# Performance work log

Hardware: AMD Instinct MI355X
Metric: run time of the kernel (lower is better)

The kernel has to match this reference:

```python
import jax, jax.numpy as jnp
import numpy as np

B, D, T = 8, 1024, 512
HID, NH, NL = 256, 4, 2
OUT = HID // NH  # 64 per-head dim
ALPHA = 0.2      # leaky relu slope
EPS = 1e-5       # layernorm eps


def setup_inputs() -> dict:
    key = jax.random.key(0)
    ks = jax.random.split(key, 10)
    X_obs = jax.random.normal(ks[0], (B, D, T), dtype=jnp.float32)
    mask = (jax.random.uniform(ks[1], (B, D, T)) < 0.8).astype(jnp.float32)
    W_in = jax.random.normal(ks[2], (2 * T, HID), dtype=jnp.float32) * (1.0 / np.sqrt(2 * T))
    b_in = jnp.zeros((HID,), dtype=jnp.float32)
    gat_W = jax.random.normal(ks[3], (NL, NH, HID, OUT), dtype=jnp.float32) * (1.0 / np.sqrt(HID))
    gat_a = jax.random.normal(ks[4], (NL, NH, 2 * OUT), dtype=jnp.float32) * 0.1
    ln_g = jnp.ones((NL, HID), dtype=jnp.float32)
    ln_b = jnp.zeros((NL, HID), dtype=jnp.float32)
    W_out = jax.random.normal(ks[5], (HID, T), dtype=jnp.float32) * (1.0 / np.sqrt(HID))
    b_out = jnp.zeros((T,), dtype=jnp.float32)
    return dict(X_obs=X_obs, mask=mask, W_in=W_in, b_in=b_in, gat_W=gat_W,
                gat_a=gat_a, ln_g=ln_g, ln_b=ln_b, W_out=W_out, b_out=b_out)


def _layer_norm(x, g, b):
    mu = jnp.mean(x, axis=-1, keepdims=True)
    var = jnp.mean((x - mu) ** 2, axis=-1, keepdims=True)
    return (x - mu) * jax.lax.rsqrt(var + EPS) * g + b


def _gat_forward(X_obs, mask, W_in, b_in, gat_W, gat_a, ln_g, ln_b, W_out, b_out):
    # mean-impute per (d, t) position across batch
    obs_sum = jnp.sum(X_obs * mask, axis=0, keepdims=True)
    obs_cnt = jnp.sum(mask, axis=0, keepdims=True)
    pos_mean = obs_sum / (obs_cnt + 1e-10)
    X_mean = X_obs * mask + (1.0 - mask) * pos_mean

    x = jnp.concatenate([X_mean, mask], axis=-1)       # (B, D, 2T)
    h = x @ W_in + b_in                                 # (B, N, HID)

    for l in range(NL):
        Wl = gat_W[l]                                   # (H, HID, OUT)
        a_left = gat_a[l, :, :OUT]                      # (H, OUT)
        a_right = gat_a[l, :, OUT:]                     # (H, OUT)
        hW = jnp.einsum('bnd,hde->bhne', h, Wl)         # (B, H, N, OUT)
        # e_ij = leakyrelu(a_left . h_i + a_right . h_j) -- avoids O(N^2 * 2d) concat
        s_l = jnp.einsum('bhne,he->bhn', hW, a_left)
        s_r = jnp.einsum('bhne,he->bhn', hW, a_right)
        e = jax.nn.leaky_relu(s_l[..., :, None] + s_r[..., None, :], ALPHA)  # (B,H,N,N)
        attn = jax.nn.softmax(e, axis=-1)
        head_out = jnp.einsum('bhnm,bhme->bhne', attn, hW)                   # (B,H,N,OUT)
        h_new = jnp.transpose(head_out, (0, 2, 1, 3)).reshape(h.shape[0], h.shape[1], HID)
        h = _layer_norm(h + h_new, ln_g[l], ln_b[l])

    return h @ W_out + b_out                            # (B, D, T)


def reference(X_obs, mask, W_in, b_in, gat_W, gat_a, ln_g, ln_b, W_out, b_out):
    return _gat_forward(X_obs, mask, W_in, b_in, gat_W, gat_a, ln_g, ln_b, W_out, b_out)
```

## Files before the change

### kernel.cpp

```cpp
#include <hip/hip_runtime.h>
#include <hip/hip_bf16.h>

constexpr int B_   = 8;
constexpr int D_   = 1024;
constexpr int T_   = 512;
constexpr int HID_ = 256;
constexpr int NH_  = 4;
constexpr int NL_  = 2;
constexpr float ALPHA_ = 0.2f;
constexpr float EPS_   = 1e-5f;
constexpr float LOG2E_ = 1.4426950408889634f;
constexpr int OUT_ = 64;
constexpr int M_ = B_ * D_;
constexpr int DT_ = D_ * T_;
constexpr int KIN_ = 2 * T_;

typedef __attribute__((ext_vector_type(8))) short short8;
typedef __attribute__((ext_vector_type(4))) float floatx4;

__device__ __forceinline__ unsigned short f2bf(float f) {
    unsigned int u = __float_as_uint(f);
    unsigned int r = u + 0x7fffu + ((u >> 16) & 1u);
    return (unsigned short)(r >> 16);
}
__device__ __forceinline__ float bf2f(unsigned short u) {
    return __uint_as_float((unsigned int)u << 16);
}
__device__ __forceinline__ unsigned int kenc(float f) {
    unsigned int u = __float_as_uint(f);
    return (u & 0x80000000u) ? ~u : (u | 0x80000000u);
}
__device__ __forceinline__ float kdec(unsigned int k) {
    unsigned int u = (k & 0x80000000u) ? (k ^ 0x80000000u) : ~k;
    return __uint_as_float(u);
}

__global__ __launch_bounds__(256) void prep_k(const float* __restrict__ X,
                                              const float* __restrict__ Mk,
                                              const float* __restrict__ W_in,
                                              const float* __restrict__ gatW,
                                              const float* __restrict__ W_out,
                                              unsigned short* __restrict__ Ain,
                                              unsigned short* __restrict__ Wt_in,
                                              unsigned short* __restrict__ Wcat,
                                              unsigned short* __restrict__ WtO,
                                              unsigned int* __restrict__ rmaxkey) {
    int bx = blockIdx.x;
    if (bx < 512) {
        int idx4 = (bx * 256 + threadIdx.x) * 4;
        int t = idx4 & (T_ - 1);
        int d = idx4 >> 9;
        float4 x[B_], m[B_];
        float4 s = {0, 0, 0, 0}, c = {0, 0, 0, 0};
#pragma unroll
        for (int b = 0; b < B_; b++) {
            x[b] = *(const float4*)&X[(size_t)b * DT_ + idx4];
            m[b] = *(const float4*)&Mk[(size_t)b * DT_ + idx4];
            s.x += x[b].x * m[b].x; s.y += x[b].y * m[b].y;
            s.z += x[b].z * m[b].z; s.w += x[b].w * m[b].w;
            c.x += m[b].x; c.y += m[b].y; c.z += m[b].z; c.w += m[b].w;
        }
        float4 pm;
        pm.x = s.x / (c.x + 1e-10f); pm.y = s.y / (c.y + 1e-10f);
        pm.z = s.z / (c.z + 1e-10f); pm.w = s.w / (c.w + 1e-10f);
#pragma unroll
        for (int b = 0; b < B_; b++) {
            size_t row = (size_t)b * D_ + d;
            ushort4 xm, mk;
            xm.x = f2bf(x[b].x * m[b].x + (1.f - m[b].x) * pm.x);
            xm.y = f2bf(x[b].y * m[b].y + (1.f - m[b].y) * pm.y);
            xm.z = f2bf(x[b].z * m[b].z + (1.f - m[b].z) * pm.z);
            xm.w = f2bf(x[b].w * m[b].w + (1.f - m[b].w) * pm.w);
            mk.x = f2bf(m[b].x); mk.y = f2bf(m[b].y);
            mk.z = f2bf(m[b].z); mk.w = f2bf(m[b].w);
            *(ushort4*)&Ain[row * KIN_ + t]      = xm;
            *(ushort4*)&Ain[row * KIN_ + T_ + t] = mk;
        }
    } else {
        int idx = (bx - 512) * 256 + threadIdx.x;
        if (idx < 64) rmaxkey[idx] = 0u;
        if (idx < 262144) {
            int n = idx >> 10, k = idx & 1023;
            Wt_in[idx] = f2bf(W_in[(size_t)k * HID_ + n]);
        } else if (idx < 393216) {
            int j = idx - 262144;
            int l = j >> 16, n = (j >> 8) & 255, k = j & 255;
            int h = n >> 6, e = n & 63;
            Wcat[j] = f2bf(gatW[(((size_t)(l * NH_ + h) * HID_) + k) * OUT_ + e]);
        } else {
            int j = idx - 393216;
            int n = j >> 8, k = j & 255;
            WtO[j] = f2bf(W_out[(size_t)k * T_ + n]);
        }
    }
}

template <int MODE>
__global__ __launch_bounds__(256) void gemm_bf16_k(
        const unsigned short* __restrict__ A,
        const unsigned short* __restrict__ Bt,
        const float* __restrict__ bias,
        float* __restrict__ C,
        unsigned short* __restrict__ Cb,
        const float* __restrict__ ga,
        float* __restrict__ s_l,
        float* __restrict__ s_r,
        unsigned int* __restrict__ rmaxkey,
        int Nsz, int Ksz) {
    __shared__ __align__(16) unsigned short As[2][64 * 72];
    __shared__ __align__(16) unsigned short Bs[2][64 * 72];
    int tid = threadIdx.x;
    int wave = tid >> 6, lane = tid & 63;
    int q = lane >> 4, r16 = lane & 15;
    int rowbase = blockIdx.y * 64;
    int colbase = blockIdx.x * 64;

    int srow = tid >> 3, sk = (tid & 7) * 8;
    const unsigned short* Ap0 = A + (size_t)(rowbase + srow) * Ksz + sk;
    const unsigned short* Ap1 = A + (size_t)(rowbase + srow + 32) * Ksz + sk;
    const unsigned short* Bp0 = Bt + (size_t)(colbase + srow) * Ksz + sk;
    const unsigned short* Bp1 = Bt + (size_t)(colbase + srow + 32) * Ksz + sk;
    int la0 = srow * 72 + sk, la1 = (srow + 32) * 72 + sk;

    floatx4 acc[4];
#pragma unroll
    for (int i = 0; i < 4; i++) acc[i] = (floatx4)0.f;

    uint4 pa0 = *(const uint4*)Ap0, pa1 = *(const uint4*)Ap1;
    uint4 pb0 = *(const uint4*)Bp0, pb1 = *(const uint4*)Bp1;
    *(uint4*)&As[0][la0] = pa0;
    *(uint4*)&As[0][la1] = pa1;
    *(uint4*)&Bs[0][la0] = pb0;
    *(uint4*)&Bs[0][la1] = pb1;

    int nk = Ksz >> 6;
    for (int it = 0; it < nk; it++) {
        int cur = it & 1;
        __syncthreads();
        if (it + 1 < nk) {
            int kt = (it + 1) << 6;
            pa0 = *(const uint4*)(Ap0 + kt);
            pa1 = *(const uint4*)(Ap1 + kt);
            pb0 = *(const uint4*)(Bp0 + kt);
            pb1 = *(const uint4*)(Bp1 + kt);
        }
#pragma unroll
        for (int t = 0; t < 2; t++) {
            short8 a = *(const short8*)&As[cur][(wave * 16 + r16) * 72 + t * 32 + q * 8];
#pragma unroll
            for (int ni = 0; ni < 4; ni++) {
                short8 b = *(const short8*)&Bs[cur][(ni * 16 + r16) * 72 + t * 32 + q * 8];
                acc[ni] = __builtin_amdgcn_mfma_f32_16x16x32_bf16(a, b, acc[ni], 0, 0, 0);
            }
        }
        if (it + 1 < nk) {
            int nxt = cur ^ 1;
            *(uint4*)&As[nxt][la0] = pa0;
            *(uint4*)&As[nxt][la1] = pa1;
            *(uint4*)&Bs[nxt][la0] = pb0;
            *(uint4*)&Bs[nxt][la1] = pb1;
        }
    }
    if constexpr (MODE == 2) {
        int bhh = ((rowbase >> 10) << 2) + blockIdx.x;
        int nb = (rowbase & (D_ - 1)) + wave * 16;
#pragma unroll
        for (int ni = 0; ni < 4; ni++) {
            int e = ni * 16 + r16;
            ushort4 pk;
            pk.x = f2bf(acc[ni][0]);
            pk.y = f2bf(acc[ni][1]);
            pk.z = f2bf(acc[ni][2]);
            pk.w = f2bf(acc[ni][3]);
            *(ushort4*)&Cb[((size_t)(bhh * 64 + e) << 10) + nb + q * 4] = pk;
        }
        const float* gab = ga + blockIdx.x * 2 * OUT_;
        float al4[4], ar4[4];
#pragma unroll
        for (int ni = 0; ni < 4; ni++) {
            al4[ni] = gab[ni * 16 + r16];
            ar4[ni] = gab[OUT_ + ni * 16 + r16];
        }
        float slv[4], srv[4];
#pragma unroll
        for (int rr = 0; rr < 4; rr++) {
            float s1 = 0.f, s2 = 0.f;
#pragma unroll
            for (int ni = 0; ni < 4; ni++) {
                s1 += acc[ni][rr] * al4[ni];
                s2 += acc[ni][rr] * ar4[ni];
            }
            slv[rr] = s1;
            srv[rr] = s2;
        }
#pragma unroll
        for (int off = 1; off < 16; off <<= 1) {
#pragma unroll
            for (int rr = 0; rr < 4; rr++) {
                slv[rr] += __shfl_xor(slv[rr], off, 64);
                srv[rr] += __shfl_xor(srv[rr], off, 64);
            }
        }
        {
            int rsel = r16 & 3;
            float sv = (rsel == 0) ? slv[0] : (rsel == 1) ? slv[1] : (rsel == 2) ? slv[2] : slv[3];
            float rv = (rsel == 0) ? srv[0] : (rsel == 1) ? srv[1] : (rsel == 2) ? srv[2] : srv[3];
            int n = nb + q * 4 + rsel;
            if (r16 < 4)                 s_l[bhh * D_ + n] = sv;
            else if (r16 >= 8 && r16 < 12) s_r[bhh * D_ + n] = rv;
        }
        float mx = fmaxf(fmaxf(srv[0], srv[1]), fmaxf(srv[2], srv[3]));
        mx = fmaxf(mx, __shfl_xor(mx, 16, 64));
        mx = fmaxf(mx, __shfl_xor(mx, 32, 64));
        if (lane == 0) atomicMax(&rmaxkey[bhh], kenc(mx));
    } else {
#pragma unroll
        for (int rr = 0; rr < 4; rr++) {
            int row = rowbase + wave * 16 + q * 4 + rr;
#pragma unroll
            for (int ni = 0; ni < 4; ni++) {
                int col = colbase + ni * 16 + r16;
                float v = acc[ni][rr] + (bias ? bias[col] : 0.f);
                if constexpr (MODE == 0) C[(size_t)row * Nsz + col] = v;
                else                     Cb[(size_t)row * Nsz + col] = f2bf(v);
            }
        }
    }
}

__global__ __launch_bounds__(256) void attn_k(const unsigned short* __restrict__ hwT,
                                              const float* __restrict__ sl_g,
                                              const float* __restrict__ sr_g,
                                              const unsigned int* __restrict__ rmaxkey,
                                              float* __restrict__ pacc,
                                              float* __restrict__ pden) {
    int bh = blockIdx.x;
    int b = bh >> 2, h = bh & 3;
    int half = blockIdx.z;
    int mb = half * 512;
    int tid = threadIdx.x;
    int wave = tid >> 6, lane = tid & 63;
    int q = lane >> 4, r16 = lane & 15;

    __shared__ float srs[512];
    __shared__ __align__(16) unsigned short Vt[2][64][136];

    {
        float2 sv = *(const float2*)&sr_g[bh * D_ + mb + tid * 2];
        sv.x *= LOG2E_; sv.y *= LOG2E_;
        *(float2*)&srs[tid * 2] = sv;
    }

    float rm = kdec(rmaxkey[bh]) * LOG2E_;
    int row0 = blockIdx.y * 64 + wave * 16;
    float sl = sl_g[bh * D_ + row0 + r16] * LOG2E_;
    float xm = sl + rm;
    float Mn = fmaxf(xm, ALPHA_ * xm);

    floatx4 acc[4];
#pragma unroll
    for (int i = 0; i < 4; i++) acc[i] = (floatx4)0.f;
    float dsum = 0.f;

    const unsigned short* vbase = hwT + ((size_t)(bh * 64) << 10) + mb;
    int se[4], sp[4];
#pragma unroll
    for (int i = 0; i < 4; i++) {
        int s = tid + i * 256;
        se[i] = s >> 4;
        sp[i] = (s & 15) * 8;
    }

    uint4 pre[4];
#pragma unroll
    for (int i = 0; i < 4; i++)
        pre[i] = *(const uint4*)&vbase[((size_t)se[i] << 10) + sp[i]];
#pragma unroll
    for (int i = 0; i < 4; i++)
        *(uint4*)&Vt[0][se[i]][sp[i]] = pre[i];
    __syncthreads();

    for (int c = 0; c < 4; c++) {
        int cur = c & 1;
        if (c < 3) {
            int mo = (c + 1) * 128;
#pragma unroll
            for (int i = 0; i < 4; i++)
                pre[i] = *(const uint4*)&vbase[((size_t)se[i] << 10) + mo + sp[i]];
        }
#pragma unroll
        for (int kk = 0; kk < 128; kk += 32) {
            int m0 = c * 128 + kk + q * 8;
            float4 s0 = *(const float4*)&srs[m0];
            float4 s1 = *(const float4*)&srs[m0 + 4];
            float sr8[8] = {s0.x, s0.y, s0.z, s0.w, s1.x, s1.y, s1.z, s1.w};
            float p[8];
#pragma unroll
            for (int j = 0; j < 8; j++) {
                float x = sl + sr8[j];
                float e = fmaxf(x, ALPHA_ * x);
                float pj = exp2f(e - Mn);
                dsum += pj;
                p[j] = pj;
            }
            union { unsigned int u[4]; short8 s8; } cv;
#pragma unroll
            for (int j = 0; j < 4; j++) {
                unsigned int lo = (__float_as_uint(p[2 * j]) + 0x8000u) >> 16;
                unsigned int hi = (__float_as_uint(p[2 * j + 1]) + 0x8000u) & 0xffff0000u;
                cv.u[j] = hi | lo;
            }
#pragma unroll
            for (int ni = 0; ni < 4; ni++) {
                short8 bfr = *(const short8*)&Vt[cur][ni * 16 + r16][kk + q * 8];
                acc[ni] = __builtin_amdgcn_mfma_f32_16x16x32_bf16(cv.s8, bfr, acc[ni], 0, 0, 0);
            }
        }
        if (c < 3) {
#pragma unroll
            for (int i = 0; i < 4; i++)
                *(uint4*)&Vt[cur ^ 1][se[i]][sp[i]] = pre[i];
        }
        __syncthreads();
    }
    dsum += __shfl_xor(dsum, 16);
    dsum += __shfl_xor(dsum, 32);
    size_t gr0 = (size_t)b * D_ + row0;
    if (lane < 16) pden[((size_t)half * M_ + gr0 + r16) * NH_ + h] = dsum;
#pragma unroll
    for (int rr = 0; rr < 4; rr++) {
        size_t grow = gr0 + q * 4 + rr;
#pragma unroll
        for (int ni = 0; ni < 4; ni++) {
            pacc[((size_t)half * M_ + grow) * HID_ + h * OUT_ + ni * 16 + r16] = acc[ni][rr];
        }
    }
}

__global__ __launch_bounds__(256) void addln_k(unsigned short* __restrict__ hbf,
                                               const float* __restrict__ pacc,
                                               const float* __restrict__ pden,
                                               const float* __restrict__ g,
                                               const float* __restrict__ bb) {
    int wave = threadIdx.x >> 6, lane = threadIdx.x & 63;
    size_t row = (size_t)blockIdx.x * 4 + wave;
    ushort4 hb = *(const ushort4*)&hbf[row * HID_ + lane * 4];
    float4 p0 = *(const float4*)&pacc[row * HID_ + lane * 4];
    float4 p1 = *(const float4*)&pacc[((size_t)M_ + row) * HID_ + lane * 4];
    int hh = lane >> 4;
    float den = pden[row * NH_ + hh] + pden[((size_t)M_ + row) * NH_ + hh];
    float inv = 1.f / den;
    float4 v = {bf2f(hb.x) + (p0.x + p1.x) * inv, bf2f(hb.y) + (p0.y + p1.y) * inv,
                bf2f(hb.z) + (p0.z + p1.z) * inv, bf2f(hb.w) + (p0.w + p1.w) * inv};
    float s = v.x + v.y + v.z + v.w;
#pragma unroll
    for (int off = 1; off < 64; off <<= 1) s += __shfl_xor(s, off, 64);
    float mu = s * (1.f / HID_);
    float4 d = {v.x - mu, v.y - mu, v.z - mu, v.w - mu};
    float s2 = d.x * d.x + d.y * d.y + d.z * d.z + d.w * d.w;
#pragma unroll
    for (int off = 1; off < 64; off <<= 1) s2 += __shfl_xor(s2, off, 64);
    float rs = rsqrtf(s2 * (1.f / HID_) + EPS_);
    float4 gg = *(const float4*)&g[lane * 4];
    float4 bbv = *(const float4*)&bb[lane * 4];
    ushort4 pk;
    pk.x = f2bf(d.x * rs * gg.x + bbv.x);
    pk.y = f2bf(d.y * rs * gg.y + bbv.y);
    pk.z = f2bf(d.z * rs * gg.z + bbv.z);
    pk.w = f2bf(d.w * rs * gg.w + bbv.w);
    *(ushort4*)&hbf[row * HID_ + lane * 4] = pk;
}

extern "C" void kernel_launch(void* const* d_in, const int* in_sizes, int n_in,
                              void* d_out, int out_size, void* d_ws, size_t ws_size,
                              hipStream_t stream) {
    const float* X_obs = (const float*)d_in[0];
    const float* mask  = (const float*)d_in[1];
    const float* W_in  = (const float*)d_in[2];
    const float* b_in  = (const float*)d_in[3];
    const float* gat_W = (const float*)d_in[4];
    const float* gat_a = (const float*)d_in[5];
    const float* ln_g  = (const float*)d_in[6];
    const float* ln_b  = (const float*)d_in[7];
    const float* W_out = (const float*)d_in[8];
    const float* b_out = (const float*)d_in[9];
    float* out = (float*)d_out;

    char* base = (char*)d_ws;
    unsigned short* Ain  = (unsigned short*)base;
    unsigned short* hwT  = (unsigned short*)base;
    float* pacc = (float*)(base + (4u << 20));
    float* pden = (float*)(base + (20u << 20));
    unsigned short* hbf   = (unsigned short*)(base + (21u << 20));
    unsigned short* Wt_in = (unsigned short*)(base + (25u << 20));
    unsigned short* Wcat  = Wt_in + (size_t)HID_ * KIN_;
    unsigned short* WtO   = Wcat + (size_t)NL_ * HID_ * HID_;
    float* slb = (float*)(WtO + (size_t)T_ * HID_);
    float* srb = slb + B_ * NH_ * D_;
    unsigned int* rmaxkey = (unsigned int*)(srb + B_ * NH_ * D_);

    prep_k<<<2560, 256, 0, stream>>>(X_obs, mask, W_in, gat_W, W_out,
                                     Ain, Wt_in, Wcat, WtO, rmaxkey);

    gemm_bf16_k<1><<<dim3(HID_ / 64, M_ / 64), 256, 0, stream>>>(
        Ain, Wt_in, b_in, nullptr, hbf, nullptr, nullptr, nullptr, nullptr,
        HID_, KIN_);

    for (int l = 0; l < NL_; l++) {
        gemm_bf16_k<2><<<dim3(HID_ / 64, M_ / 64), 256, 0, stream>>>(
            hbf, Wcat + (size_t)l * HID_ * HID_, nullptr, nullptr, hwT,
            gat_a + (size_t)l * NH_ * 2 * OUT_, slb, srb, rmaxkey + l * 32,
            HID_, HID_);
        attn_k<<<dim3(B_ * NH_, D_ / 64, 2), 256, 0, stream>>>(
            hwT, slb, srb, rmaxkey + l * 32, pacc, pden);
        addln_k<<<M_ / 4, 256, 0, stream>>>(hbf, pacc, pden,
                                            ln_g + (size_t)l * HID_,
                                            ln_b + (size_t)l * HID_);
    }

    gemm_bf16_k<0><<<dim3(T_ / 64, M_ / 64), 256, 0, stream>>>(
        hbf, WtO, b_out, out, nullptr, nullptr, nullptr, nullptr, nullptr,
        T_, HID_);
}
```

Baseline: 219.2 us.

## Fuse residual add and layernorm into following GEMM prologue, drop addln kernel

Removes the separate add+layernorm kernel. Each GAT layer's residual+LN is now computed in the prologue of the next GEMM (the layer-2 projection and the output projection), with the normalized tile staged straight into shared memory. The K=256 GEMMs now load the whole A and B tiles into LDS at once instead of double-buffering. Each column block recomputes LN for its rows, which is redundant work (4x or 8x), and only blockIdx.x==0 writes the normalized h out to a ping-pong buffer.

```diff
diff --git a/kernel.cpp b/kernel.cpp
--- a/kernel.cpp
+++ b/kernel.cpp
@@ -95,18 +95,11 @@
     }
 }
 
-template <int MODE>
-__global__ __launch_bounds__(256) void gemm_bf16_k(
+__global__ __launch_bounds__(256) void gemm1_k(
         const unsigned short* __restrict__ A,
         const unsigned short* __restrict__ Bt,
         const float* __restrict__ bias,
-        float* __restrict__ C,
-        unsigned short* __restrict__ Cb,
-        const float* __restrict__ ga,
-        float* __restrict__ s_l,
-        float* __restrict__ s_r,
-        unsigned int* __restrict__ rmaxkey,
-        int Nsz, int Ksz) {
+        unsigned short* __restrict__ Cb) {
     __shared__ __align__(16) unsigned short As[2][64 * 72];
     __shared__ __align__(16) unsigned short Bs[2][64 * 72];
     int tid = threadIdx.x;
@@ -116,10 +109,10 @@
     int colbase = blockIdx.x * 64;
 
     int srow = tid >> 3, sk = (tid & 7) * 8;
-    const unsigned short* Ap0 = A + (size_t)(rowbase + srow) * Ksz + sk;
-    const unsigned short* Ap1 = A + (size_t)(rowbase + srow + 32) * Ksz + sk;
-    const unsigned short* Bp0 = Bt + (size_t)(colbase + srow) * Ksz + sk;
-    const unsigned short* Bp1 = Bt + (size_t)(colbase + srow + 32) * Ksz + sk;
+    const unsigned short* Ap0 = A + (size_t)(rowbase + srow) * KIN_ + sk;
+    const unsigned short* Ap1 = A + (size_t)(rowbase + srow + 32) * KIN_ + sk;
+    const unsigned short* Bp0 = Bt + (size_t)(colbase + srow) * KIN_ + sk;
+    const unsigned short* Bp1 = Bt + (size_t)(colbase + srow + 32) * KIN_ + sk;
     int la0 = srow * 72 + sk, la1 = (srow + 32) * 72 + sk;
 
     floatx4 acc[4];
@@ -133,11 +126,10 @@
     *(uint4*)&Bs[0][la0] = pb0;
     *(uint4*)&Bs[0][la1] = pb1;
 
-    int nk = Ksz >> 6;
-    for (int it = 0; it < nk; it++) {
+    for (int it = 0; it < 16; it++) {
         int cur = it & 1;
         __syncthreads();
-        if (it + 1 < nk) {
+        if (it + 1 < 16) {
             int kt = (it + 1) << 6;
             pa0 = *(const uint4*)(Ap0 + kt);
             pa1 = *(const uint4*)(Ap1 + kt);
@@ -153,7 +145,7 @@
                 acc[ni] = __builtin_amdgcn_mfma_f32_16x16x32_bf16(a, b, acc[ni], 0, 0, 0);
             }
         }
-        if (it + 1 < nk) {
+        if (it + 1 < 16) {
             int nxt = cur ^ 1;
             *(uint4*)&As[nxt][la0] = pa0;
             *(uint4*)&As[nxt][la1] = pa1;
@@ -161,7 +153,109 @@
             *(uint4*)&Bs[nxt][la1] = pb1;
         }
     }
-    if constexpr (MODE == 2) {
+#pragma unroll
+    for (int rr = 0; rr < 4; rr++) {
+        int row = rowbase + wave * 16 + q * 4 + rr;
+#pragma unroll
+        for (int ni = 0; ni < 4; ni++) {
+            int col = colbase + ni * 16 + r16;
+            Cb[(size_t)row * HID_ + col] = f2bf(acc[ni][rr] + bias[col]);
+        }
+    }
+}
+
+template <bool LNF, int EPI>
+__global__ __launch_bounds__(256) void gemm_small_k(
+        const unsigned short* __restrict__ Ah,
+        const float* __restrict__ pacc,
+        const float* __restrict__ pden,
+        const float* __restrict__ lng,
+        const float* __restrict__ lnb,
+        unsigned short* __restrict__ hOut,
+        const unsigned short* __restrict__ Bt,
+        const float* __restrict__ bias,
+        float* __restrict__ C,
+        unsigned short* __restrict__ hwT,
+        const float* __restrict__ ga,
+        float* __restrict__ s_l,
+        float* __restrict__ s_r,
+        unsigned int* __restrict__ rmaxkey,
+        int Nsz) {
+    constexpr int STR = 264;
+    __shared__ __align__(16) unsigned short As[64 * STR];
+    __shared__ __align__(16) unsigned short Bs[64 * STR];
+    int tid = threadIdx.x;
+    int wave = tid >> 6, lane = tid & 63;
+    int q = lane >> 4, r16 = lane & 15;
+    int rowbase = blockIdx.y * 64;
+    int colbase = blockIdx.x * 64;
+
+#pragma unroll
+    for (int i = 0; i < 8; i++) {
+        int s = tid + i * 256;
+        int n = s >> 5, part = s & 31;
+        *(uint4*)&Bs[n * STR + part * 8] =
+            *(const uint4*)&Bt[(size_t)(colbase + n) * HID_ + part * 8];
+    }
+    if constexpr (!LNF) {
+#pragma unroll
+        for (int i = 0; i < 8; i++) {
+            int s = tid + i * 256;
+            int r = s >> 5, part = s & 31;
+            *(uint4*)&As[r * STR + part * 8] =
+                *(const uint4*)&Ah[(size_t)(rowbase + r) * HID_ + part * 8];
+        }
+    } else {
+        float4 gg = *(const float4*)&lng[lane * 4];
+        float4 bbv = *(const float4*)&lnb[lane * 4];
+        int hh = lane >> 4;
+        bool wr = (hOut != nullptr) && (blockIdx.x == 0);
+#pragma unroll 4
+        for (int i = 0; i < 16; i++) {
+            size_t row = (size_t)rowbase + wave * 16 + i;
+            ushort4 hb = *(const ushort4*)&Ah[row * HID_ + lane * 4];
+            float4 p0 = *(const float4*)&pacc[row * HID_ + lane * 4];
+            float4 p1 = *(const float4*)&pacc[((size_t)M_ + row) * HID_ + lane * 4];
+            float den = pden[row * NH_ + hh] + pden[((size_t)M_ + row) * NH_ + hh];
+            float inv = 1.f / den;
+            float4 v = {bf2f(hb.x) + (p0.x + p1.x) * inv,
+                        bf2f(hb.y) + (p0.y + p1.y) * inv,
+                        bf2f(hb.z) + (p0.z + p1.z) * inv,
+                        bf2f(hb.w) + (p0.w + p1.w) * inv};
+            float s = v.x + v.y + v.z + v.w;
+#pragma unroll
+            for (int off = 1; off < 64; off <<= 1) s += __shfl_xor(s, off, 64);
+            float mu = s * (1.f / HID_);
+            float4 d = {v.x - mu, v.y - mu, v.z - mu, v.w - mu};
+            float s2 = d.x * d.x + d.y * d.y + d.z * d.z + d.w * d.w;
+#pragma unroll
+            for (int off = 1; off < 64; off <<= 1) s2 += __shfl_xor(s2, off, 64);
+            float rs = rsqrtf(s2 * (1.f / HID_) + EPS_);
+            ushort4 pk;
+            pk.x = f2bf(d.x * rs * gg.x + bbv.x);
+            pk.y = f2bf(d.y * rs * gg.y + bbv.y);
+            pk.z = f2bf(d.z * rs * gg.z + bbv.z);
+            pk.w = f2bf(d.w * rs * gg.w + bbv.w);
+            *(ushort4*)&As[(wave * 16 + i) * STR + lane * 4] = pk;
+            if (wr) *(ushort4*)&hOut[row * HID_ + lane * 4] = pk;
+        }
+    }
+    __syncthreads();
+
+    floatx4 acc[4];
+#pragma unroll
+    for (int i = 0; i < 4; i++) acc[i] = (floatx4)0.f;
+#pragma unroll
+    for (int kk = 0; kk < 8; kk++) {
+        short8 a = *(const short8*)&As[(wave * 16 + r16) * STR + kk * 32 + q * 8];
+#pragma unroll
+        for (int ni = 0; ni < 4; ni++) {
+            short8 b = *(const short8*)&Bs[(ni * 16 + r16) * STR + kk * 32 + q * 8];
+            acc[ni] = __builtin_amdgcn_mfma_f32_16x16x32_bf16(a, b, acc[ni], 0, 0, 0);
+        }
+    }
+
+    if constexpr (EPI == 2) {
         int bhh = ((rowbase >> 10) << 2) + blockIdx.x;
         int nb = (rowbase & (D_ - 1)) + wave * 16;
 #pragma unroll
@@ -172,7 +266,7 @@
             pk.y = f2bf(acc[ni][1]);
             pk.z = f2bf(acc[ni][2]);
             pk.w = f2bf(acc[ni][3]);
-            *(ushort4*)&Cb[((size_t)(bhh * 64 + e) << 10) + nb + q * 4] = pk;
+            *(ushort4*)&hwT[((size_t)(bhh * 64 + e) << 10) + nb + q * 4] = pk;
         }
         const float* gab = ga + blockIdx.x * 2 * OUT_;
         float al4[4], ar4[4];
@@ -206,7 +300,7 @@
             float sv = (rsel == 0) ? slv[0] : (rsel == 1) ? slv[1] : (rsel == 2) ? slv[2] : slv[3];
             float rv = (rsel == 0) ? srv[0] : (rsel == 1) ? srv[1] : (rsel == 2) ? srv[2] : srv[3];
             int n = nb + q * 4 + rsel;
-            if (r16 < 4)                 s_l[bhh * D_ + n] = sv;
+            if (r16 < 4)                   s_l[bhh * D_ + n] = sv;
             else if (r16 >= 8 && r16 < 12) s_r[bhh * D_ + n] = rv;
         }
         float mx = fmaxf(fmaxf(srv[0], srv[1]), fmaxf(srv[2], srv[3]));
@@ -220,9 +314,7 @@
 #pragma unroll
             for (int ni = 0; ni < 4; ni++) {
                 int col = colbase + ni * 16 + r16;
-                float v = acc[ni][rr] + (bias ? bias[col] : 0.f);
-                if constexpr (MODE == 0) C[(size_t)row * Nsz + col] = v;
-                else                     Cb[(size_t)row * Nsz + col] = f2bf(v);
+                C[(size_t)row * Nsz + col] = acc[ni][rr] + bias[col];
             }
         }
     }
@@ -335,40 +427,6 @@
             pacc[((size_t)half * M_ + grow) * HID_ + h * OUT_ + ni * 16 + r16] = acc[ni][rr];
         }
     }
-}
-
-__global__ __launch_bounds__(256) void addln_k(unsigned short* __restrict__ hbf,
-                                               const float* __restrict__ pacc,
-                                               const float* __restrict__ pden,
-                                               const float* __restrict__ g,
-                                               const float* __restrict__ bb) {
-    int wave = threadIdx.x >> 6, lane = threadIdx.x & 63;
-    size_t row = (size_t)blockIdx.x * 4 + wave;
-    ushort4 hb = *(const ushort4*)&hbf[row * HID_ + lane * 4];
-    float4 p0 = *(const float4*)&pacc[row * HID_ + lane * 4];
-    float4 p1 = *(const float4*)&pacc[((size_t)M_ + row) * HID_ + lane * 4];
-    int hh = lane >> 4;
-    float den = pden[row * NH_ + hh] + pden[((size_t)M_ + row) * NH_ + hh];
-    float inv = 1.f / den;
-    float4 v = {bf2f(hb.x) + (p0.x + p1.x) * inv, bf2f(hb.y) + (p0.y + p1.y) * inv,
-                bf2f(hb.z) + (p0.z + p1.z) * inv, bf2f(hb.w) + (p0.w + p1.w) * inv};
-    float s = v.x + v.y + v.z + v.w;
-#pragma unroll
-    for (int off = 1; off < 64; off <<= 1) s += __shfl_xor(s, off, 64);
-    float mu = s * (1.f / HID_);
-    float4 d = {v.x - mu, v.y - mu, v.z - mu, v.w - mu};
-    float s2 = d.x * d.x + d.y * d.y + d.z * d.z + d.w * d.w;
-#pragma unroll
-    for (int off = 1; off < 64; off <<= 1) s2 += __shfl_xor(s2, off, 64);
-    float rs = rsqrtf(s2 * (1.f / HID_) + EPS_);
-    float4 gg = *(const float4*)&g[lane * 4];
-    float4 bbv = *(const float4*)&bb[lane * 4];
-    ushort4 pk;
-    pk.x = f2bf(d.x * rs * gg.x + bbv.x);
-    pk.y = f2bf(d.y * rs * gg.y + bbv.y);
-    pk.z = f2bf(d.z * rs * gg.z + bbv.z);
-    pk.w = f2bf(d.w * rs * gg.w + bbv.w);
-    *(ushort4*)&hbf[row * HID_ + lane * 4] = pk;
 }
 
 extern "C" void kernel_launch(void* const* d_in, const int* in_sizes, int n_in,
@@ -391,8 +449,9 @@
     unsigned short* hwT  = (unsigned short*)base;
     float* pacc = (float*)(base + (4u << 20));
     float* pden = (float*)(base + (20u << 20));
-    unsigned short* hbf   = (unsigned short*)(base + (21u << 20));
-    unsigned short* Wt_in = (unsigned short*)(base + (25u << 20));
+    unsigned short* hbfA  = (unsigned short*)(base + (21u << 20));
+    unsigned short* hbfB  = (unsigned short*)(base + (25u << 20));
+    unsigned short* Wt_in = (unsigned short*)(base + (29u << 20));
     unsigned short* Wcat  = Wt_in + (size_t)HID_ * KIN_;
     unsigned short* WtO   = Wcat + (size_t)NL_ * HID_ * HID_;
     float* slb = (float*)(WtO + (size_t)T_ * HID_);
@@ -402,23 +461,22 @@
     prep_k<<<2560, 256, 0, stream>>>(X_obs, mask, W_in, gat_W, W_out,
                                      Ain, Wt_in, Wcat, WtO, rmaxkey);
 
-    gemm_bf16_k<1><<<dim3(HID_ / 64, M_ / 64), 256, 0, stream>>>(
-        Ain, Wt_in, b_in, nullptr, hbf, nullptr, nullptr, nullptr, nullptr,
-        HID_, KIN_);
-
-    for (int l = 0; l < NL_; l++) {
-        gemm_bf16_k<2><<<dim3(HID_ / 64, M_ / 64), 256, 0, stream>>>(
-            hbf, Wcat + (size_t)l * HID_ * HID_, nullptr, nullptr, hwT,
-            gat_a + (size_t)l * NH_ * 2 * OUT_, slb, srb, rmaxkey + l * 32,
-            HID_, HID_);
-        attn_k<<<dim3(B_ * NH_, D_ / 64, 2), 256, 0, stream>>>(
-            hwT, slb, srb, rmaxkey + l * 32, pacc, pden);
-        addln_k<<<M_ / 4, 256, 0, stream>>>(hbf, pacc, pden,
-                                            ln_g + (size_t)l * HID_,
-                                            ln_b + (size_t)l * HID_);
-    }
-
-    gemm_bf16_k<0><<<dim3(T_ / 64, M_ / 64), 256, 0, stream>>>(
-        hbf, WtO, b_out, out, nullptr, nullptr, nullptr, nullptr, nullptr,
-        T_, HID_);
-}
+    gemm1_k<<<dim3(HID_ / 64, M_ / 64), 256, 0, stream>>>(Ain, Wt_in, b_in, hbfA);
+
+    gemm_small_k<false, 2><<<dim3(HID_ / 64, M_ / 64), 256, 0, stream>>>(
+        hbfA, nullptr, nullptr, nullptr, nullptr, nullptr,
+        Wcat, nullptr, nullptr, hwT, gat_a, slb, srb, rmaxkey, HID_);
+    attn_k<<<dim3(B_ * NH_, D_ / 64, 2), 256, 0, stream>>>(
+        hwT, slb, srb, rmaxkey, pacc, pden);
+
+    gemm_small_k<true, 2><<<dim3(HID_ / 64, M_ / 64), 256, 0, stream>>>(
+        hbfA, pacc, pden, ln_g, ln_b, hbfB,
+        Wcat + (size_t)HID_ * HID_, nullptr, nullptr, hwT,
+        gat_a + (size_t)NH_ * 2 * OUT_, slb, srb, rmaxkey + 32, HID_);
+    attn_k<<<dim3(B_ * NH_, D_ / 64, 2), 256, 0, stream>>>(
+        hwT, slb, srb, rmaxkey + 32, pacc, pden);
+
+    gemm_small_k<true, 0><<<dim3(T_ / 64, M_ / 64), 256, 0, stream>>>(
+        hbfB, pacc, pden, ln_g + HID_, ln_b + HID_, nullptr,
+        WtO, b_out, out, nullptr, nullptr, nullptr, nullptr, nullptr, T_);
+}
```

Result: slower. 249.1 us (+13.6%).
